# Performance work log

Hardware: AMD Instinct MI355X
Metric: run time of the kernel (lower is better)

The kernel has to match this reference:

```python
import jax, jax.numpy as jnp
import numpy as np

B, S, H = 32, 2048, 1024
STDV = 0.1


def setup_inputs() -> dict:
    key = jax.random.key(0)
    ks = jax.random.split(key, 8)
    u = lambda k, shape: jax.random.uniform(k, shape, minval=-STDV, maxval=STDV, dtype=jnp.float32)
    return {
        "inputs": jax.random.normal(ks[0], (B, S, H), dtype=jnp.float32),
        "qvector": jax.random.normal(ks[1], (B, H), dtype=jnp.float32),
        "W_u_1": u(ks[2], (H, H)),
        "W_u_m_1": u(ks[3], (H, H)),
        "W_u_h_1": u(ks[4], (H, 1)),
        "W_u_2": u(ks[5], (H, H)),
        "W_u_m_2": u(ks[6], (H, H)),
        "W_u_h_2": u(ks[7], (H, 1)),
    }


def reference(inputs, qvector, W_u_1, W_u_m_1, W_u_h_1, W_u_2, W_u_m_2, W_u_h_2):
    # inputs: [B, S, H], qvector: [B, H]
    def hop(m, W, Wm, Wh):
        # M = tanh(inputs @ W) gated by tanh(m @ Wm)  -> [B, S, H]
        M = jnp.tanh(jnp.einsum("bsh,hd->bsd", inputs, W))
        M = M * jnp.tanh(m @ Wm)[:, None, :]
        U = jnp.einsum("bsd,do->bso", M, Wh)        # [B, S, 1]
        alpha = jax.nn.softmax(U, axis=1)           # softmax over sequence
        return jnp.sum(inputs * alpha, axis=1)      # [B, H]

    mean_in = jnp.mean(inputs, axis=1)              # [B, H]
    u_att0 = mean_in
    m0 = mean_in * qvector
    u_att1 = hop(m0, W_u_1, W_u_m_1, W_u_h_1)
    m1 = m0 + u_att0 * qvector
    u_att2 = hop(m1, W_u_2, W_u_m_2, W_u_h_2)
    # original returns list [u_att0, u_att1, u_att2]; stack for a single array
    return jnp.stack([u_att0, u_att1, u_att2])      # [3, B, H]
```

## Files before the change

kernel.cpp:

```cpp
#include <hip/hip_runtime.h>
#include <hip/hip_bf16.h>
#include <math.h>

#define B_  32
#define S_  2048
#define H_  1024
#define M_TOT (B_ * S_)

typedef __bf16 bf16x8 __attribute__((ext_vector_type(8)));
typedef float  f32x4  __attribute__((ext_vector_type(4)));

__device__ __forceinline__ unsigned short f2bf(float f) {
    union { float f; unsigned int u; } v; v.f = f;
    unsigned int u = v.u;
    return (unsigned short)((u + 0x7fffu + ((u >> 16) & 1u)) >> 16);
}

__device__ __forceinline__ float bf2f(unsigned short s) {
    return __uint_as_float(((unsigned int)s) << 16);
}

__device__ __forceinline__ float fast_tanh(float x) {
    float e = __expf(2.0f * x);
    return 1.0f - 2.0f / (e + 1.0f);
}

__global__ void k_meanconv(const float* __restrict__ x,
                           unsigned short* __restrict__ xbf,
                           float* __restrict__ meanOut ) {
    int b  = blockIdx.x;
    int sc = blockIdx.y;
    int t  = threadIdx.x;
    size_t base = ((size_t)b * S_ + (size_t)sc * 32) * H_;
    const float4* xr = (const float4*)(x + base);
    ushort4* xo = (ushort4*)(xbf + base);
    float a0 = 0.f, a1 = 0.f, a2 = 0.f, a3 = 0.f;
    for (int s = 0; s < 32; ++s) {
        float4 v = xr[(size_t)s * 256 + t];
        a0 += v.x; a1 += v.y; a2 += v.z; a3 += v.w;
        ushort4 o;
        o.x = f2bf(v.x); o.y = f2bf(v.y); o.z = f2bf(v.z); o.w = f2bf(v.w);
        xo[(size_t)s * 256 + t] = o;
    }
    const float scl = 1.0f / (float)S_;
    float* mp = meanOut + b * H_ + t * 4;
    atomicAdd(mp + 0, a0 * scl);
    atomicAdd(mp + 1, a1 * scl);
    atomicAdd(mp + 2, a2 * scl);
    atomicAdd(mp + 3, a3 * scl);
}

__global__ void k_wconv(const float* __restrict__ W1,
                        const float* __restrict__ W2,
                        unsigned short* __restrict__ WT) {
    int n = blockIdx.x;
    int t = threadIdx.x;
    const float* src = (n < H_) ? (W1 + n) : (W2 + (n - H_));
    unsigned short* dst = WT + (size_t)n * H_;
    for (int kk = 0; kk < 4; ++kk) {
        int k = t + kk * 256;
        dst[k] = f2bf(src[(size_t)k * H_]);
    }
}

__global__ void k_vpart(const float* __restrict__ meanIn,
                        const float* __restrict__ q,
                        const float* __restrict__ Wm1,
                        const float* __restrict__ Wm2,
                        float* __restrict__ vtmp ) {
    int b   = blockIdx.x;
    int hop = blockIdx.y;
    int hc  = blockIdx.z;
    int t   = threadIdx.x;
    __shared__ float mL[128];
    float scale = (hop == 0) ? 1.0f : 2.0f;
    int h0 = hc * 128;
    if (t < 128)
        mL[t] = meanIn[b * H_ + h0 + t] * q[b * H_ + h0 + t] * scale;
    __syncthreads();
    const float* Wm = hop ? Wm2 : Wm1;
    int d0 = t * 4;
    float a0 = 0.f, a1 = 0.f, a2 = 0.f, a3 = 0.f;
    for (int h = 0; h < 128; ++h) {
        float m = mL[h];
        float4 w = *(const float4*)(Wm + (size_t)(h0 + h) * H_ + d0);
        a0 += m * w.x; a1 += m * w.y; a2 += m * w.z; a3 += m * w.w;
    }
    float* vo = vtmp + b * 2048 + hop * H_ + d0;
    atomicAdd(vo + 0, a0);
    atomicAdd(vo + 1, a1);
    atomicAdd(vo + 2, a2);
    atomicAdd(vo + 3, a3);
}

__global__ void k_vfin(const float* __restrict__ vtmp,
                       const float* __restrict__ Wh1,
                       const float* __restrict__ Wh2,
                       float* __restrict__ vcat) {
    int i = blockIdx.x * 256 + threadIdx.x;
    int hop = (i >> 10) & 1;
    int d = i & 1023;
    const float* Wh = hop ? Wh2 : Wh1;
    vcat[i] = tanhf(vtmp[i]) * Wh[d];
}

__global__ __launch_bounds__(512, 2) void k_gemm(const unsigned short* __restrict__ Xbf,
                                                 const unsigned short* __restrict__ WT,
                                                 const float* __restrict__ vcat,
                                                 float* __restrict__ U ) {
    int raw = blockIdx.x;
    int wg  = (raw & 7) * 256 + (raw >> 3);
    int nt = wg & 7;
    int mt = wg >> 3;
    int m0 = mt * 256;
    int n0 = nt * 256;

    int t    = threadIdx.x;
    int lane = t & 63;
    int wave = t >> 6;
    int wm = wave >> 2;
    int wn = wave & 3;
    int fr = lane & 15;
    int fq = lane >> 4;
    int s0 = (fq + fr) & 7;

    __shared__ unsigned short lds[2][2][256 * 64];

    const unsigned short* gA[4];
    const unsigned short* gB[4];
#pragma unroll
    for (int L = 0; L < 4; ++L) {
        int idx  = L * 512 + t;
        int row  = idx >> 3;
        int cst  = idx & 7;
        int csrc = (cst - row) & 7;
        gA[L] = Xbf + (size_t)(m0 + row) * H_ + csrc * 8;
        gB[L] = WT  + (size_t)(n0 + row) * H_ + csrc * 8;
    }

#define STG_A(buf_, L_, v_) __builtin_amdgcn_global_load_lds( \
        (const __attribute__((address_space(1))) void*)(gA[L_] + (v_) * 64), \
        (__attribute__((address_space(3))) void*)(&lds[buf_][0][(L_) * 4096 + t * 8]), 16, 0, 0)
#define STG_B(buf_, L_, v_) __builtin_amdgcn_global_load_lds( \
        (const __attribute__((address_space(1))) void*)(gB[L_] + (v_) * 64), \
        (__attribute__((address_space(3))) void*)(&lds[buf_][1][(L_) * 4096 + t * 8]), 16, 0, 0)

#define ARD(buf_, QM_, i_, kk_) \
    (*(const bf16x8*)&lds[buf_][0][(wm * 128 + (QM_) * 64 + (i_) * 16 + fr) * 64 + (s0 ^ ((kk_) * 4)) * 8])
#define BRD(buf_, QN_, j_, kk_) \
    (*(const bf16x8*)&lds[buf_][1][(wn * 64 + (QN_) * 32 + (j_) * 16 + fr) * 64 + (s0 ^ ((kk_) * 4)) * 8])

    int b   = m0 >> 11;
    int hop = n0 >> 10;
    float vv[4];
#pragma unroll
    for (int j = 0; j < 4; ++j)
        vv[j] = vcat[b * 2048 + n0 + wn * 64 + j * 16 + fr];

    f32x4 acc[8][4];
#pragma unroll
    for (int i = 0; i < 8; ++i)
#pragma unroll
        for (int j = 0; j < 4; ++j)
#pragma unroll
            for (int r = 0; r < 4; ++r) acc[i][j][r] = 0.0f;

    STG_A(0, 0, 0); STG_A(0, 1, 0); STG_A(0, 2, 0); STG_A(0, 3, 0);
    STG_B(0, 0, 0); STG_B(0, 1, 0); STG_B(0, 2, 0); STG_B(0, 3, 0);
    STG_A(1, 0, 1); STG_A(1, 1, 1); STG_A(1, 2, 1); STG_A(1, 3, 1);
    STG_B(1, 0, 1); STG_B(1, 1, 1); STG_B(1, 2, 1); STG_B(1, 3, 1);
    asm volatile("s_waitcnt vmcnt(8)" ::: "memory");
    __builtin_amdgcn_s_barrier();
    __builtin_amdgcn_sched_barrier(0);

    bf16x8 a[4][2];
    bf16x8 b0[2][2], b1[2][2];

#pragma unroll 2
    for (int v = 0; v < 16; ++v) {
        int cur = v & 1;
        bool sN2 = (v <= 13);

#pragma unroll
        for (int i = 0; i < 4; ++i) { a[i][0] = ARD(cur, 0, i, 0); a[i][1] = ARD(cur, 0, i, 1); }
#pragma unroll
        for (int j = 0; j < 2; ++j) { b0[j][0] = BRD(cur, 0, j, 0); b0[j][1] = BRD(cur, 0, j, 1); }
        __builtin_amdgcn_sched_barrier(0);
        __builtin_amdgcn_s_barrier();
        asm volatile("s_waitcnt lgkmcnt(0)" ::: "memory");
        __builtin_amdgcn_sched_barrier(0);
        __builtin_amdgcn_s_setprio(1);
#pragma unroll
        for (int i = 0; i < 4; ++i)
#pragma unroll
            for (int j = 0; j < 2; ++j) {
                acc[i][j] = __builtin_amdgcn_mfma_f32_16x16x32_bf16(a[i][0], b0[j][0], acc[i][j], 0, 0, 0);
                acc[i][j] = __builtin_amdgcn_mfma_f32_16x16x32_bf16(a[i][1], b0[j][1], acc[i][j], 0, 0, 0);
            }
        __builtin_amdgcn_s_setprio(0);
        __builtin_amdgcn_s_barrier();

#pragma unroll
        for (int j = 0; j < 2; ++j) { b1[j][0] = BRD(cur, 1, j, 0); b1[j][1] = BRD(cur, 1, j, 1); }
        if (sN2) { STG_A(cur, 0, v + 2); STG_A(cur, 2, v + 2); }
        __builtin_amdgcn_sched_barrier(0);
        __builtin_amdgcn_s_barrier();
        asm volatile("s_waitcnt lgkmcnt(0)" ::: "memory");
        __builtin_amdgcn_sched_barrier(0);
        __builtin_amdgcn_s_setprio(1);
#pragma unroll
        for (int i = 0; i < 4; ++i)
#pragma unroll
            for (int j = 0; j < 2; ++j) {
                acc[i][2 + j] = __builtin_amdgcn_mfma_f32_16x16x32_bf16(a[i][0], b1[j][0], acc[i][2 + j], 0, 0, 0);
                acc[i][2 + j] = __builtin_amdgcn_mfma_f32_16x16x32_bf16(a[i][1], b1[j][1], acc[i][2 + j], 0, 0, 0);
            }
        __builtin_amdgcn_s_setprio(0);
        __builtin_amdgcn_s_barrier();

#pragma unroll
        for (int i = 0; i < 4; ++i) { a[i][0] = ARD(cur, 1, i, 0); a[i][1] = ARD(cur, 1, i, 1); }
        if (sN2) { STG_B(cur, 0, v + 2); STG_B(cur, 1, v + 2); }
        __builtin_amdgcn_sched_barrier(0);
        __builtin_amdgcn_s_barrier();
        asm volatile("s_waitcnt lgkmcnt(0)" ::: "memory");
        __builtin_amdgcn_sched_barrier(0);
        __builtin_amdgcn_s_setprio(1);
#pragma unroll
        for (int i = 0; i < 4; ++i)
#pragma unroll
            for (int j = 0; j < 2; ++j) {
                acc[4 + i][j] = __builtin_amdgcn_mfma_f32_16x16x32_bf16(a[i][0], b0[j][0], acc[4 + i][j], 0, 0, 0);
                acc[4 + i][j] = __builtin_amdgcn_mfma_f32_16x16x32_bf16(a[i][1], b0[j][1], acc[4 + i][j], 0, 0, 0);
            }
        __builtin_amdgcn_s_setprio(0);
        __builtin_amdgcn_s_barrier();

        if (sN2) { STG_B(cur, 2, v + 2); STG_B(cur, 3, v + 2); STG_A(cur, 1, v + 2); STG_A(cur, 3, v + 2); }
        __builtin_amdgcn_sched_barrier(0);
        __builtin_amdgcn_s_barrier();
        __builtin_amdgcn_s_setprio(1);
#pragma unroll
        for (int i = 0; i < 4; ++i)
#pragma unroll
            for (int j = 0; j < 2; ++j) {
                acc[4 + i][2 + j] = __builtin_amdgcn_mfma_f32_16x16x32_bf16(a[i][0], b1[j][0], acc[4 + i][2 + j], 0, 0, 0);
                acc[4 + i][2 + j] = __builtin_amdgcn_mfma_f32_16x16x32_bf16(a[i][1], b1[j][1], acc[4 + i][2 + j], 0, 0, 0);
            }
        __builtin_amdgcn_s_setprio(0);
        if (sN2) { asm volatile("s_waitcnt vmcnt(8)" ::: "memory"); }
        else     { asm volatile("s_waitcnt vmcnt(0)" ::: "memory"); }
        __builtin_amdgcn_s_barrier();
        __builtin_amdgcn_sched_barrier(0);
    }

#pragma unroll
    for (int i8 = 0; i8 < 8; ++i8) {
#pragma unroll
        for (int r = 0; r < 4; ++r) {
            float sum = fast_tanh(acc[i8][0][r]) * vv[0]
                      + fast_tanh(acc[i8][1][r]) * vv[1]
                      + fast_tanh(acc[i8][2][r]) * vv[2]
                      + fast_tanh(acc[i8][3][r]) * vv[3];
            sum += __shfl_xor(sum, 1);
            sum += __shfl_xor(sum, 2);
            sum += __shfl_xor(sum, 4);
            sum += __shfl_xor(sum, 8);
            if (fr == 0) {
                int row = m0 + wm * 128 + i8 * 16 + fq * 4 + r;
                atomicAdd(&U[(size_t)hop * M_TOT + row], sum);
            }
        }
    }
#undef STG_A
#undef STG_B
#undef ARD
#undef BRD
}

__global__ void k_softmax(const float* __restrict__ U, float* __restrict__ alpha) {
    int id  = blockIdx.x;
    int hop = id >> 5, b = id & 31;
    int t = threadIdx.x;
    const float* u = U + (size_t)hop * M_TOT + (size_t)b * S_;
    float* al = alpha + (size_t)hop * M_TOT + (size_t)b * S_;
    float v[8];
    float mx = -1e30f;
#pragma unroll
    for (int i = 0; i < 8; ++i) { v[i] = u[t + i * 256]; mx = fmaxf(mx, v[i]); }
    __shared__ float red[256];
    red[t] = mx; __syncthreads();
    for (int s = 128; s > 0; s >>= 1) {
        if (t < s) red[t] = fmaxf(red[t], red[t + s]);
        __syncthreads();
    }
    mx = red[0]; __syncthreads();
    float sum = 0.f;
#pragma unroll
    for (int i = 0; i < 8; ++i) { v[i] = expf(v[i] - mx); sum += v[i]; }
    red[t] = sum; __syncthreads();
    for (int s = 128; s > 0; s >>= 1) {
        if (t < s) red[t] += red[t + s];
        __syncthreads();
    }
    float inv = 1.0f / red[0];
#pragma unroll
    for (int i = 0; i < 8; ++i) al[t + i * 256] = v[i] * inv;
}

__global__ void k_wsum(const unsigned short* __restrict__ Xbf,
                       const float* __restrict__ alpha,
                       float* __restrict__ out1 ,
                       float* __restrict__ out2 ) {
    int b  = blockIdx.x;
    int sc = blockIdx.y;
    int t  = threadIdx.x;
    __shared__ float a1[32], a2[32];
    int s0 = sc * 32;
    if (t < 32)       a1[t]      = alpha[(size_t)b * S_ + s0 + t];
    else if (t < 64)  a2[t - 32] = alpha[(size_t)M_TOT + (size_t)b * S_ + s0 + (t - 32)];
    __syncthreads();
    const ushort4* xr = (const ushort4*)(Xbf + ((size_t)b * S_ + s0) * H_);
    float x0a = 0.f, x1a = 0.f, x2a = 0.f, x3a = 0.f;
    float x0b = 0.f, x1b = 0.f, x2b = 0.f, x3b = 0.f;
    for (int s = 0; s < 32; ++s) {
        ushort4 u = xr[(size_t)s * 256 + t];
        float f0 = bf2f(u.x), f1 = bf2f(u.y), f2 = bf2f(u.z), f3 = bf2f(u.w);
        float w1 = a1[s], w2 = a2[s];
        x0a += f0 * w1; x1a += f1 * w1; x2a += f2 * w1; x3a += f3 * w1;
        x0b += f0 * w2; x1b += f1 * w2; x2b += f2 * w2; x3b += f3 * w2;
    }
    float* o1 = out1 + b * H_ + t * 4;
    float* o2 = out2 + b * H_ + t * 4;
    atomicAdd(o1 + 0, x0a); atomicAdd(o1 + 1, x1a);
    atomicAdd(o1 + 2, x2a); atomicAdd(o1 + 3, x3a);
    atomicAdd(o2 + 0, x0b); atomicAdd(o2 + 1, x1b);
    atomicAdd(o2 + 2, x2b); atomicAdd(o2 + 3, x3b);
}

extern "C" void kernel_launch(void* const* d_in, const int* in_sizes, int n_in,
                              void* d_out, int out_size, void* d_ws, size_t ws_size,
                              hipStream_t stream) {
    const float* inputs = (const float*)d_in[0];
    const float* q      = (const float*)d_in[1];
    const float* W1     = (const float*)d_in[2];
    const float* Wm1    = (const float*)d_in[3];
    const float* Wh1    = (const float*)d_in[4];
    const float* W2     = (const float*)d_in[5];
    const float* Wm2    = (const float*)d_in[6];
    const float* Wh2    = (const float*)d_in[7];
    float* out = (float*)d_out;

    char* ws = (char*)d_ws;
    unsigned short* Xbf  = (unsigned short*)(ws);
    unsigned short* WT   = (unsigned short*)(ws + 134217728);
    float*          vcat = (float*)(ws + 138412032);
    float*          U    = (float*)(ws + 138674176);
    float*          alph = (float*)(ws + 139198464);
    float*          vtmp = (float*)(ws + 139722752);

    hipMemsetAsync(d_out, 0, (size_t)out_size * sizeof(float), stream);
    hipMemsetAsync(U, 0, 524288 + 524288 + 262144, stream);

    k_meanconv<<<dim3(32, 64), 256, 0, stream>>>(inputs, Xbf, out);
    k_wconv  <<<dim3(2048),    256, 0, stream>>>(W1, W2, WT);
    k_vpart  <<<dim3(32, 2, 8), 256, 0, stream>>>(out, q, Wm1, Wm2, vtmp);
    k_vfin   <<<dim3(256),     256, 0, stream>>>(vtmp, Wh1, Wh2, vcat);
    k_gemm   <<<dim3(2048),    512, 0, stream>>>(Xbf, WT, vcat, U);
    k_softmax<<<dim3(64),      256, 0, stream>>>(U, alph);
    k_wsum   <<<dim3(32, 64),  256, 0, stream>>>(Xbf, alph, out + 32768, out + 65536);
}
```

Baseline: 843.5 us.

## Restructure GEMM main loop into single-barrier double buffer with register prefetch

Replaces the multi-phase ping-pong loop, which had many s_barriers per K-step and prefetched two steps ahead, with a simpler double buffer. Each iteration issues all global-to-LDS loads for the next step up front and synchronizes once with __syncthreads. The A/B fragments for the next step are read from LDS into separate registers (a0/a1) before the last MFMA block, and per-row global pointers are collapsed into a single base pointer to save registers. This aims to cut barrier overhead, but reducing the prefetch distance from two steps to one may expose more memory latency and raise register pressure.

```diff
diff --git a/kernel.cpp b/kernel.cpp
--- a/kernel.cpp
+++ b/kernel.cpp
@@ -126,23 +126,16 @@
 
     __shared__ unsigned short lds[2][2][256 * 64];
 
-    const unsigned short* gA[4];
-    const unsigned short* gB[4];
-#pragma unroll
-    for (int L = 0; L < 4; ++L) {
-        int idx  = L * 512 + t;
-        int row  = idx >> 3;
-        int cst  = idx & 7;
-        int csrc = (cst - row) & 7;
-        gA[L] = Xbf + (size_t)(m0 + row) * H_ + csrc * 8;
-        gB[L] = WT  + (size_t)(n0 + row) * H_ + csrc * 8;
-    }
+    int rowt = t >> 3;
+    int csrc = ((t & 7) - rowt) & 7;
+    const unsigned short* gA0 = Xbf + (size_t)(m0 + rowt) * H_ + csrc * 8;
+    const unsigned short* gB0 = WT  + (size_t)(n0 + rowt) * H_ + csrc * 8;
 
 #define STG_A(buf_, L_, v_) __builtin_amdgcn_global_load_lds( \
-        (const __attribute__((address_space(1))) void*)(gA[L_] + (v_) * 64), \
+        (const __attribute__((address_space(1))) void*)(gA0 + (size_t)(L_) * 64 * H_ + (v_) * 64), \
         (__attribute__((address_space(3))) void*)(&lds[buf_][0][(L_) * 4096 + t * 8]), 16, 0, 0)
 #define STG_B(buf_, L_, v_) __builtin_amdgcn_global_load_lds( \
-        (const __attribute__((address_space(1))) void*)(gB[L_] + (v_) * 64), \
+        (const __attribute__((address_space(1))) void*)(gB0 + (size_t)(L_) * 64 * H_ + (v_) * 64), \
         (__attribute__((address_space(3))) void*)(&lds[buf_][1][(L_) * 4096 + t * 8]), 16, 0, 0)
 
 #define ARD(buf_, QM_, i_, kk_) \
@@ -150,6 +143,8 @@
 #define BRD(buf_, QN_, j_, kk_) \
     (*(const bf16x8*)&lds[buf_][1][(wn * 64 + (QN_) * 32 + (j_) * 16 + fr) * 64 + (s0 ^ ((kk_) * 4)) * 8])
 
+#define MFMA(a_, b_, c_) __builtin_amdgcn_mfma_f32_16x16x32_bf16(a_, b_, c_, 0, 0, 0)
+
     int b   = m0 >> 11;
     int hop = n0 >> 10;
     float vv[4];
@@ -167,91 +162,69 @@
 
     STG_A(0, 0, 0); STG_A(0, 1, 0); STG_A(0, 2, 0); STG_A(0, 3, 0);
     STG_B(0, 0, 0); STG_B(0, 1, 0); STG_B(0, 2, 0); STG_B(0, 3, 0);
-    STG_A(1, 0, 1); STG_A(1, 1, 1); STG_A(1, 2, 1); STG_A(1, 3, 1);
-    STG_B(1, 0, 1); STG_B(1, 1, 1); STG_B(1, 2, 1); STG_B(1, 3, 1);
-    asm volatile("s_waitcnt vmcnt(8)" ::: "memory");
-    __builtin_amdgcn_s_barrier();
-    __builtin_amdgcn_sched_barrier(0);
-
-    bf16x8 a[4][2];
-    bf16x8 b0[2][2], b1[2][2];
+    __syncthreads();
+
+    bf16x8 a0[4][2], a1[4][2], b0[2][2], b1[2][2];
+#pragma unroll
+    for (int i = 0; i < 4; ++i) { a0[i][0] = ARD(0, 0, i, 0); a0[i][1] = ARD(0, 0, i, 1); }
+#pragma unroll
+    for (int j = 0; j < 2; ++j) { b0[j][0] = BRD(0, 0, j, 0); b0[j][1] = BRD(0, 0, j, 1); }
 
 #pragma unroll 2
     for (int v = 0; v < 16; ++v) {
-        int cur = v & 1;
-        bool sN2 = (v <= 13);
-
-#pragma unroll
-        for (int i = 0; i < 4; ++i) { a[i][0] = ARD(cur, 0, i, 0); a[i][1] = ARD(cur, 0, i, 1); }
-#pragma unroll
-        for (int j = 0; j < 2; ++j) { b0[j][0] = BRD(cur, 0, j, 0); b0[j][1] = BRD(cur, 0, j, 1); }
-        __builtin_amdgcn_sched_barrier(0);
-        __builtin_amdgcn_s_barrier();
-        asm volatile("s_waitcnt lgkmcnt(0)" ::: "memory");
-        __builtin_amdgcn_sched_barrier(0);
+        const int cur = v & 1;
+        const int nxt = cur ^ 1;
+        if (v < 15) {
+            STG_A(nxt, 0, v + 1); STG_A(nxt, 1, v + 1); STG_A(nxt, 2, v + 1); STG_A(nxt, 3, v + 1);
+            STG_B(nxt, 0, v + 1); STG_B(nxt, 1, v + 1); STG_B(nxt, 2, v + 1); STG_B(nxt, 3, v + 1);
+        }
+#pragma unroll
+        for (int j = 0; j < 2; ++j) { b1[j][0] = BRD(cur, 1, j, 0); b1[j][1] = BRD(cur, 1, j, 1); }
         __builtin_amdgcn_s_setprio(1);
 #pragma unroll
         for (int i = 0; i < 4; ++i)
 #pragma unroll
             for (int j = 0; j < 2; ++j) {
-                acc[i][j] = __builtin_amdgcn_mfma_f32_16x16x32_bf16(a[i][0], b0[j][0], acc[i][j], 0, 0, 0);
-                acc[i][j] = __builtin_amdgcn_mfma_f32_16x16x32_bf16(a[i][1], b0[j][1], acc[i][j], 0, 0, 0);
+                acc[i][j] = MFMA(a0[i][0], b0[j][0], acc[i][j]);
+                acc[i][j] = MFMA(a0[i][1], b0[j][1], acc[i][j]);
             }
         __builtin_amdgcn_s_setprio(0);
-        __builtin_amdgcn_s_barrier();
-
-#pragma unroll
-        for (int j = 0; j < 2; ++j) { b1[j][0] = BRD(cur, 1, j, 0); b1[j][1] = BRD(cur, 1, j, 1); }
-        if (sN2) { STG_A(cur, 0, v + 2); STG_A(cur, 2, v + 2); }
-        __builtin_amdgcn_sched_barrier(0);
-        __builtin_amdgcn_s_barrier();
-        asm volatile("s_waitcnt lgkmcnt(0)" ::: "memory");
-        __builtin_amdgcn_sched_barrier(0);
+#pragma unroll
+        for (int i = 0; i < 4; ++i) { a1[i][0] = ARD(cur, 1, i, 0); a1[i][1] = ARD(cur, 1, i, 1); }
         __builtin_amdgcn_s_setprio(1);
 #pragma unroll
         for (int i = 0; i < 4; ++i)
 #pragma unroll
             for (int j = 0; j < 2; ++j) {
-                acc[i][2 + j] = __builtin_amdgcn_mfma_f32_16x16x32_bf16(a[i][0], b1[j][0], acc[i][2 + j], 0, 0, 0);
-                acc[i][2 + j] = __builtin_amdgcn_mfma_f32_16x16x32_bf16(a[i][1], b1[j][1], acc[i][2 + j], 0, 0, 0);
+                acc[i][2 + j] = MFMA(a0[i][0], b1[j][0], acc[i][2 + j]);
+                acc[i][2 + j] = MFMA(a0[i][1], b1[j][1], acc[i][2 + j]);
             }
         __builtin_amdgcn_s_setprio(0);
-        __builtin_amdgcn_s_barrier();
-
-#pragma unroll
-        for (int i = 0; i < 4; ++i) { a[i][0] = ARD(cur, 1, i, 0); a[i][1] = ARD(cur, 1, i, 1); }
-        if (sN2) { STG_B(cur, 0, v + 2); STG_B(cur, 1, v + 2); }
-        __builtin_amdgcn_sched_barrier(0);
-        __builtin_amdgcn_s_barrier();
-        asm volatile("s_waitcnt lgkmcnt(0)" ::: "memory");
-        __builtin_amdgcn_sched_barrier(0);
         __builtin_amdgcn_s_setprio(1);
 #pragma unroll
         for (int i = 0; i < 4; ++i)
 #pragma unroll
             for (int j = 0; j < 2; ++j) {
-                acc[4 + i][j] = __builtin_amdgcn_mfma_f32_16x16x32_bf16(a[i][0], b0[j][0], acc[4 + i][j], 0, 0, 0);
-                acc[4 + i][j] = __builtin_amdgcn_mfma_f32_16x16x32_bf16(a[i][1], b0[j][1], acc[4 + i][j], 0, 0, 0);
+                acc[4 + i][j] = MFMA(a1[i][0], b0[j][0], acc[4 + i][j]);
+                acc[4 + i][j] = MFMA(a1[i][1], b0[j][1], acc[4 + i][j]);
             }
         __builtin_amdgcn_s_setprio(0);
-        __builtin_amdgcn_s_barrier();
-
-        if (sN2) { STG_B(cur, 2, v + 2); STG_B(cur, 3, v + 2); STG_A(cur, 1, v + 2); STG_A(cur, 3, v + 2); }
-        __builtin_amdgcn_sched_barrier(0);
-        __builtin_amdgcn_s_barrier();
+        if (v < 15) __syncthreads();
+        if (v < 15) {
+#pragma unroll
+            for (int i = 0; i < 4; ++i) { a0[i][0] = ARD(nxt, 0, i, 0); a0[i][1] = ARD(nxt, 0, i, 1); }
+#pragma unroll
+            for (int j = 0; j < 2; ++j) { b0[j][0] = BRD(nxt, 0, j, 0); b0[j][1] = BRD(nxt, 0, j, 1); }
+        }
         __builtin_amdgcn_s_setprio(1);
 #pragma unroll
         for (int i = 0; i < 4; ++i)
 #pragma unroll
             for (int j = 0; j < 2; ++j) {
-                acc[4 + i][2 + j] = __builtin_amdgcn_mfma_f32_16x16x32_bf16(a[i][0], b1[j][0], acc[4 + i][2 + j], 0, 0, 0);
-                acc[4 + i][2 + j] = __builtin_amdgcn_mfma_f32_16x16x32_bf16(a[i][1], b1[j][1], acc[4 + i][2 + j], 0, 0, 0);
+                acc[4 + i][2 + j] = MFMA(a1[i][0], b1[j][0], acc[4 + i][2 + j]);
+                acc[4 + i][2 + j] = MFMA(a1[i][1], b1[j][1], acc[4 + i][2 + j]);
             }
         __builtin_amdgcn_s_setprio(0);
-        if (sN2) { asm volatile("s_waitcnt vmcnt(8)" ::: "memory"); }
-        else     { asm volatile("s_waitcnt vmcnt(0)" ::: "memory"); }
-        __builtin_amdgcn_s_barrier();
-        __builtin_amdgcn_sched_barrier(0);
     }
 
 #pragma unroll
@@ -276,6 +249,7 @@
 #undef STG_B
 #undef ARD
 #undef BRD
+#undef MFMA
 }
 
 __global__ void k_softmax(const float* __restrict__ U, float* __restrict__ alpha) {
```

Result: no change. 852.7 us (+1.1%).
